# Optimization experiments

Hardware: AMD Instinct MI355X
Metric: run time of the kernel (lower is better)

The kernel has to match this reference:

```python
import jax, jax.numpy as jnp
import numpy as np

D_MODEL = 1024
N_HEADS = 16
D_HEAD = D_MODEL // N_HEADS
ROPE_BASE = 10000.0


def setup_inputs() -> dict:
    key = jax.random.key(0)
    k1, k2, k3, k4, k5 = jax.random.split(key, 5)
    std = 0.02 / np.sqrt(2 * 12)  # scaled_xavier with n_layers=12
    x = jax.random.normal(k1, (2, 2048, D_MODEL), dtype=jnp.float32)
    qkv_w = jax.random.normal(k2, (3 * D_MODEL, D_MODEL), dtype=jnp.float32) * std
    qkv_b = jnp.zeros((3 * D_MODEL,), dtype=jnp.float32)
    proj_w = jax.random.normal(k3, (D_MODEL, D_MODEL), dtype=jnp.float32) * std
    proj_b = jnp.zeros((D_MODEL,), dtype=jnp.float32)
    return {"x": x, "qkv_w": qkv_w, "qkv_b": qkv_b, "proj_w": proj_w, "proj_b": proj_b}


def _rope_cos_sin(seq_len, dtype):
    inv_freq = 1.0 / (ROPE_BASE ** (jnp.arange(0, D_HEAD, 2, dtype=jnp.float32) / D_HEAD))
    t = jnp.arange(seq_len, dtype=jnp.float32)
    freqs = jnp.einsum("t,d->td", t, inv_freq)          # [S, Dh/2]
    freqs = jnp.concatenate([freqs, freqs], axis=-1)      # [S, Dh]
    return jnp.cos(freqs).astype(dtype), jnp.sin(freqs).astype(dtype)


def _rotate_half(x):
    x1, x2 = jnp.split(x, 2, axis=-1)
    return jnp.concatenate([-x2, x1], axis=-1)


def reference(x, qkv_w, qkv_b, proj_w, proj_b):
    B, S, D = x.shape
    H, Dh = N_HEADS, D_HEAD
    scale = 1.0 / np.sqrt(Dh)

    qkv = x @ qkv_w.T + qkv_b                              # [B, S, 3D]
    qkv = qkv.reshape(B, S, 3, H, Dh)
    q = jnp.transpose(qkv[:, :, 0], (0, 2, 1, 3))          # [B, H, S, Dh]
    k = jnp.transpose(qkv[:, :, 1], (0, 2, 1, 3))
    v = jnp.transpose(qkv[:, :, 2], (0, 2, 1, 3))

    cos, sin = _rope_cos_sin(S, x.dtype)                   # [S, Dh]
    q = q * cos + _rotate_half(q) * sin
    k = k * cos + _rotate_half(k) * sin

    scores = jnp.einsum("bhsd,bhtd->bhst", q, k) * scale   # [B, H, S, S]
    causal = jnp.triu(jnp.ones((S, S), dtype=bool), k=1)
    neg = jnp.finfo(scores.dtype).min
    scores = jnp.where(causal[None, None], neg, scores)

    probs = jax.nn.softmax(scores, axis=-1)
    ctx = jnp.einsum("bhst,bhtd->bhsd", probs, v)          # [B, H, S, Dh]
    out = jnp.transpose(ctx, (0, 2, 1, 3)).reshape(B, S, D)
    out = out @ proj_w.T + proj_b
    return out
```

## Files before the change

### kernel.cpp

```cpp
#include <hip/hip_runtime.h>
#include <hip/hip_bf16.h>

#define BATCH 2
#define SEQ   2048
#define DMODEL 1024
#define NHEADS 16
#define DHEAD  64
#define MTOT   (BATCH * SEQ)
#define QKSTR  2048

typedef __attribute__((ext_vector_type(8))) short bf16x8;
typedef __attribute__((ext_vector_type(4))) float f32x4;

__device__ __forceinline__ void glds16(const void* g, void* l)
{
    __builtin_amdgcn_global_load_lds(
        (const __attribute__((address_space(1))) unsigned int*)g,
        (__attribute__((address_space(3))) unsigned int*)l, 16, 0, 0);
}

__global__ void cast_all_kernel(
    const float* __restrict__ a, __hip_bfloat16* __restrict__ oa, int na4,
    const float* __restrict__ b, __hip_bfloat16* __restrict__ ob, int nb4,
    const float* __restrict__ c, __hip_bfloat16* __restrict__ oc, int nc4)
{
    int i = blockIdx.x * blockDim.x + threadIdx.x;
    const float* src; __hip_bfloat16* dst; int j = i;
    if (j < na4) { src = a; dst = oa; }
    else {
        j -= na4;
        if (j < nb4) { src = b; dst = ob; }
        else {
            j -= nb4;
            if (j >= nc4) return;
            src = c; dst = oc;
        }
    }
    float4 v = ((const float4*)src)[j];
    __hip_bfloat16 tmp[4];
    tmp[0] = __float2bfloat16(v.x);
    tmp[1] = __float2bfloat16(v.y);
    tmp[2] = __float2bfloat16(v.z);
    tmp[3] = __float2bfloat16(v.w);
    *(uint2*)(dst + 4 * (size_t)j) = *(const uint2*)tmp;
}

#define GTM 128
#define GBK 64

__device__ __forceinline__ void store_out(float* p, float v) { *p = v; }
__device__ __forceinline__ void store_out(__hip_bfloat16* p, float v) { *p = __float2bfloat16(v); }

template <typename OutT, int MODE, int TN>
__global__ __launch_bounds__(256) void gemm_bias_kernel(
    const __hip_bfloat16* __restrict__ A, const __hip_bfloat16* __restrict__ W,
    const float* __restrict__ bias, OutT* __restrict__ out,
    __hip_bfloat16* __restrict__ vtg,
    int M, int N, int K)
{
    const int NI = TN / 32;
    const int bm = blockIdx.x * GTM;
    const int bn = blockIdx.y * TN;
    const int tid = threadIdx.x;
    const int wave = tid >> 6;
    const int lane = tid & 63;
    const int quad = lane >> 4;
    const int l16 = lane & 15;
    const int wm = (wave & 1) * 64;
    const int wn = (wave >> 1) * (TN / 2);

    __shared__ __hip_bfloat16 As[GTM * GBK];
    __shared__ __hip_bfloat16 Bs[TN * GBK];

    f32x4 acc[4][NI] = {};

    const int srow = lane >> 3;
    const int gc8 = (((lane & 7) ^ srow)) * 8;

    for (int kt = 0; kt < K; kt += GBK) {
#pragma unroll
        for (int t = 0; t < 4; t++) {
            int i = wave * 4 + t;
            glds16(A + (size_t)(bm + i * 8 + srow) * K + kt + gc8, As + i * 512);
        }
#pragma unroll
        for (int t = 0; t < TN / 32; t++) {
            int i = wave * (TN / 32) + t;
            glds16(W + (size_t)(bn + i * 8 + srow) * K + kt + gc8, Bs + i * 512);
        }
        __syncthreads();

#pragma unroll
        for (int kk = 0; kk < 2; kk++) {
            bf16x8 af[4], bfr[NI];
#pragma unroll
            for (int i = 0; i < 4; i++) {
                int ra = wm + i * 16 + l16;
                af[i] = *(const bf16x8*)(As + ra * 64 + (((kk << 2) + quad) ^ (ra & 7)) * 8);
            }
#pragma unroll
            for (int i = 0; i < NI; i++) {
                int rb = wn + i * 16 + l16;
                bfr[i] = *(const bf16x8*)(Bs + rb * 64 + (((kk << 2) + quad) ^ (rb & 7)) * 8);
            }
#pragma unroll
            for (int mi = 0; mi < 4; mi++)
#pragma unroll
                for (int ni = 0; ni < NI; ni++)
                    acc[mi][ni] = __builtin_amdgcn_mfma_f32_16x16x32_bf16(
                        af[mi], bfr[ni], acc[mi][ni], 0, 0, 0);
        }
        __syncthreads();
    }

    if (MODE == 1 && (bn + wn) < 2 * DMODEL) {
#pragma unroll
        for (int ni = 0; ni < 2; ni++) {
            int col = bn + wn + ni * 16 + l16;
            int i32 = col & 31;
            float invf = exp2f(-13.287712379549449f * (float)i32 * (1.0f / 32.0f));
            float b1 = bias[col], b2 = bias[col + 32];
#pragma unroll
            for (int mi = 0; mi < 4; mi++) {
#pragma unroll
                for (int r = 0; r < 4; r++) {
                    int row = bm + wm + mi * 16 + quad * 4 + r;
                    int s = row & (SEQ - 1);
                    float ang = (float)s * invf;
                    float sn, cs;
                    __sincosf(ang, &sn, &cs);
                    float x1 = acc[mi][ni][r] + b1;
                    float x2 = acc[mi][ni + 2][r] + b2;
                    store_out(&out[(size_t)row * QKSTR + col], x1 * cs - x2 * sn);
                    store_out(&out[(size_t)row * QKSTR + col + 32], x2 * cs + x1 * sn);
                }
            }
        }
    } else if (MODE == 1) {
#pragma unroll
        for (int ni = 0; ni < NI; ni++) {
            int colg = bn + wn + ni * 16 + l16;
            int vcol = colg - 2 * DMODEL;
            int hh = vcol >> 6, dh = vcol & 63;
            float bv = bias[colg];
#pragma unroll
            for (int mi = 0; mi < 4; mi++) {
                int row0 = bm + wm + mi * 16 + quad * 4;
                int bb = row0 >> 11;
                int ss = row0 & (SEQ - 1);
                __hip_bfloat16 tmp[4];
#pragma unroll
                for (int r = 0; r < 4; r++)
                    tmp[r] = __float2bfloat16(acc[mi][ni][r] + bv);
                *(uint2*)(vtg + (((size_t)bb * NHEADS + hh) * DHEAD + dh) * SEQ + ss) =
                    *(uint2*)tmp;
            }
        }
    } else {
#pragma unroll
        for (int mi = 0; mi < 4; mi++)
#pragma unroll
            for (int ni = 0; ni < NI; ni++) {
                int col = bn + wn + ni * 16 + l16;
                float bv = bias[col];
#pragma unroll
                for (int r = 0; r < 4; r++) {
                    int row = bm + wm + mi * 16 + quad * 4 + r;
                    store_out(&out[(size_t)row * N + col], acc[mi][ni][r] + bv);
                }
            }
    }
}

__global__ __launch_bounds__(512, 4) void flash_attn_mfma_kernel(
    const __hip_bfloat16* __restrict__ qkb,
    const __hip_bfloat16* __restrict__ vtg,
    __hip_bfloat16* __restrict__ ctx)
{
    const int bh = blockIdx.x;
    const int b = bh >> 4, h = bh & 15;
    const int y = blockIdx.y;
    const int qa = y, qb = 31 - y;
    const int tid = threadIdx.x;
    const int w = tid >> 6;
    const int lane = tid & 63;
    const int quad = lane >> 4;
    const int l16 = lane & 15;
    const int w4 = w & 3;
    const int qt = (w >> 2) ? qb : qa;

    __shared__ __hip_bfloat16 Ks[2][64 * 64];
    __shared__ __hip_bfloat16 Vt[2][64 * 64];
    __shared__ __hip_bfloat16 Ps[128 * 64];

    const __hip_bfloat16* qbase = qkb + (size_t)b * SEQ * QKSTR + h * DHEAD;
    const __hip_bfloat16* kbase = qbase + DMODEL;
    const __hip_bfloat16* vbase = vtg + (size_t)bh * DHEAD * SEQ;

    const __hip_bfloat16* qrow = qbase + (size_t)(qt * 64 + w4 * 16 + l16) * QKSTR;
    bf16x8 qf0 = *(const bf16x8*)(qrow + quad * 8);
    bf16x8 qf1 = *(const bf16x8*)(qrow + 32 + quad * 8);

    const int srow = lane >> 3;
    const int gc8 = ((lane & 7) ^ srow) * 8;
    const __hip_bfloat16* kg = kbase + (size_t)(w * 8 + srow) * QKSTR + gc8;
    const __hip_bfloat16* vg = vbase + (size_t)(w * 8 + srow) * SEQ + gc8;

    const int xr = l16 & 7;
    const int fo0 = l16 * 64 + ((quad ^ xr) << 3);
    const int fo1 = l16 * 64 + (((4 + quad) ^ xr) << 3);
    const int pband = w * 16;
    const int pfo0 = (pband + l16) * 64 + ((quad ^ xr) << 3);
    const int pfo1 = (pband + l16) * 64 + (((4 + quad) ^ xr) << 3);

    const short onev = (l16 == 0) ? (short)0x3F80 : (short)0;
    const bf16x8 ones = {onev, onev, onev, onev, onev, onev, onev, onev};

    glds16(kg, &Ks[0][w * 512]);
    glds16(vg, &Vt[0][w * 512]);

    f32x4 oacc[5] = {};

    for (int jt = 0; jt <= qb; jt++) {
        __syncthreads();
        const int cur = jt & 1;
        if (jt < qb) {
            glds16(kg + (size_t)(jt + 1) * 64 * QKSTR, &Ks[cur ^ 1][w * 512]);
            glds16(vg + (jt + 1) * 64, &Vt[cur ^ 1][w * 512]);
        }
        if (jt <= qt) {
            const __hip_bfloat16* ks = Ks[cur];
            const __hip_bfloat16* vs = Vt[cur];

            f32x4 s4[4] = {};
#pragma unroll
            for (int nt = 0; nt < 4; nt++)
                s4[nt] = __builtin_amdgcn_mfma_f32_16x16x32_bf16(
                    qf0, *(const bf16x8*)(ks + nt * 1024 + fo0), s4[nt], 0, 0, 0);
#pragma unroll
            for (int nt = 0; nt < 4; nt++)
                s4[nt] = __builtin_amdgcn_mfma_f32_16x16x32_bf16(
                    qf1, *(const bf16x8*)(ks + nt * 1024 + fo1), s4[nt], 0, 0, 0);

            const bool diag = (jt == qt);
#pragma unroll
            for (int nt = 0; nt < 4; nt++)
#pragma unroll
                for (int r = 0; r < 4; r++) {
                    float p = __expf(s4[nt][r] * 0.125f);
                    if (diag)
                        p = (nt * 16 + l16 <= w4 * 16 + quad * 4 + r) ? p : 0.f;
                    int rr = quad * 4 + r;
                    Ps[(pband + rr) * 64 +
                       (((nt * 2 + (l16 >> 3)) ^ (rr & 7)) << 3) + xr] =
                        __float2bfloat16(p);
                }

            bf16x8 pf0 = *(const bf16x8*)(Ps + pfo0);
            bf16x8 pf1 = *(const bf16x8*)(Ps + pfo1);
#pragma unroll
            for (int dt = 0; dt < 4; dt++)
                oacc[dt] = __builtin_amdgcn_mfma_f32_16x16x32_bf16(
                    pf0, *(const bf16x8*)(vs + dt * 1024 + fo0), oacc[dt], 0, 0, 0);
            oacc[4] = __builtin_amdgcn_mfma_f32_16x16x32_bf16(pf0, ones, oacc[4], 0, 0, 0);
#pragma unroll
            for (int dt = 0; dt < 4; dt++)
                oacc[dt] = __builtin_amdgcn_mfma_f32_16x16x32_bf16(
                    pf1, *(const bf16x8*)(vs + dt * 1024 + fo1), oacc[dt], 0, 0, 0);
            oacc[4] = __builtin_amdgcn_mfma_f32_16x16x32_bf16(pf1, ones, oacc[4], 0, 0, 0);
        }
    }

#pragma unroll
    for (int r = 0; r < 4; r++) {
        float lv = __shfl(oacc[4][r], lane & 48);
        float il = 1.0f / lv;
        int qg = qt * 64 + w4 * 16 + quad * 4 + r;
        __hip_bfloat16* op = ctx + (((size_t)b * SEQ + qg) * NHEADS + h) * DHEAD + l16;
#pragma unroll
        for (int dt = 0; dt < 4; dt++)
            op[dt * 16] = __float2bfloat16(oacc[dt][r] * il);
    }
}

extern "C" void kernel_launch(void* const* d_in, const int* in_sizes, int n_in,
                              void* d_out, int out_size, void* d_ws, size_t ws_size,
                              hipStream_t stream)
{
    const float* x      = (const float*)d_in[0];
    const float* qkv_w  = (const float*)d_in[1];
    const float* qkv_b  = (const float*)d_in[2];
    const float* proj_w = (const float*)d_in[3];
    const float* proj_b = (const float*)d_in[4];
    float* out = (float*)d_out;

    char* w = (char*)d_ws;
    __hip_bfloat16* qkb = (__hip_bfloat16*)w;  w += (size_t)MTOT * QKSTR * 2;
    __hip_bfloat16* vtg = (__hip_bfloat16*)w;  w += (size_t)MTOT * DMODEL * 2;
    __hip_bfloat16* ctx = (__hip_bfloat16*)w;  w += (size_t)MTOT * DMODEL * 2;
    __hip_bfloat16* xb  = (__hip_bfloat16*)w;  w += (size_t)MTOT * DMODEL * 2;
    __hip_bfloat16* wqk = (__hip_bfloat16*)w;  w += (size_t)3 * DMODEL * DMODEL * 2;
    __hip_bfloat16* wpr = (__hip_bfloat16*)w;

    const int na4 = MTOT * DMODEL / 4;
    const int nb4 = 3 * DMODEL * DMODEL / 4;
    const int nc4 = DMODEL * DMODEL / 4;

    cast_all_kernel<<<(na4 + nb4 + nc4 + 255) / 256, 256, 0, stream>>>(
        x, xb, na4, qkv_w, wqk, nb4, proj_w, wpr, nc4);

    gemm_bias_kernel<__hip_bfloat16, 1, 128>
        <<<dim3(MTOT / GTM, (3 * DMODEL) / 128), 256, 0, stream>>>(
        xb, wqk, qkv_b, qkb, vtg, MTOT, 3 * DMODEL, DMODEL);

    flash_attn_mfma_kernel<<<dim3(BATCH * NHEADS, 16), 512, 0, stream>>>(qkb, vtg, ctx);

    gemm_bias_kernel<float, 0, 64>
        <<<dim3(MTOT / GTM, DMODEL / 64), 256, 0, stream>>>(
        ctx, wpr, proj_b, out, nullptr, MTOT, DMODEL, DMODEL);
}
```

Baseline: 183.6 us.

## Double-buffer GEMM LDS tiles with K=32 steps to overlap loads and MFMA

The bias GEMM now stages A and W tiles in two LDS buffers of depth 32 along K, with a matching XOR swizzle. The loads for the next tile are issued before the MFMAs on the current tile, and one barrier per iteration replaces the previous two. This is meant to hide global-to-LDS latency behind compute. In exchange the K loop runs twice as many iterations with less work per barrier, and there is less MFMA work available to cover each load.

```diff
diff --git a/kernel.cpp b/kernel.cpp
--- a/kernel.cpp
+++ b/kernel.cpp
@@ -46,7 +46,6 @@
 }
 
 #define GTM 128
-#define GBK 64
 
 __device__ __forceinline__ void store_out(float* p, float v) { *p = v; }
 __device__ __forceinline__ void store_out(__hip_bfloat16* p, float v) { *p = __float2bfloat16(v); }
@@ -69,48 +68,73 @@
     const int wm = (wave & 1) * 64;
     const int wn = (wave >> 1) * (TN / 2);
 
-    __shared__ __hip_bfloat16 As[GTM * GBK];
-    __shared__ __hip_bfloat16 Bs[TN * GBK];
+    __shared__ __hip_bfloat16 As[2][GTM * 32];
+    __shared__ __hip_bfloat16 Bs[2][TN * 32];
 
     f32x4 acc[4][NI] = {};
 
-    const int srow = lane >> 3;
-    const int gc8 = (((lane & 7) ^ srow)) * 8;
-
-    for (int kt = 0; kt < K; kt += GBK) {
-#pragma unroll
-        for (int t = 0; t < 4; t++) {
-            int i = wave * 4 + t;
-            glds16(A + (size_t)(bm + i * 8 + srow) * K + kt + gc8, As + i * 512);
-        }
-#pragma unroll
-        for (int t = 0; t < TN / 32; t++) {
-            int i = wave * (TN / 32) + t;
-            glds16(W + (size_t)(bn + i * 8 + srow) * K + kt + gc8, Bs + i * 512);
-        }
+    const int r16 = lane >> 2;
+    const int gco = ((lane & 3) ^ (r16 & 3)) * 8;
+
+    const int fo = ((quad ^ (l16 & 3)) << 3);
+
+    const int niter = K >> 5;
+
+    {
+#pragma unroll
+        for (int c = 0; c < 2; c++) {
+            int br = wave * 32 + c * 16;
+            glds16(A + (size_t)(bm + br + r16) * K + gco, &As[0][br * 32]);
+        }
+        if (TN == 128) {
+#pragma unroll
+            for (int c = 0; c < 2; c++) {
+                int br = wave * 32 + c * 16;
+                glds16(W + (size_t)(bn + br + r16) * K + gco, &Bs[0][br * 32]);
+            }
+        } else {
+            int br = wave * 16;
+            glds16(W + (size_t)(bn + br + r16) * K + gco, &Bs[0][br * 32]);
+        }
+    }
+
+    for (int it = 0; it < niter; it++) {
         __syncthreads();
-
-#pragma unroll
-        for (int kk = 0; kk < 2; kk++) {
-            bf16x8 af[4], bfr[NI];
-#pragma unroll
-            for (int i = 0; i < 4; i++) {
-                int ra = wm + i * 16 + l16;
-                af[i] = *(const bf16x8*)(As + ra * 64 + (((kk << 2) + quad) ^ (ra & 7)) * 8);
-            }
-#pragma unroll
-            for (int i = 0; i < NI; i++) {
-                int rb = wn + i * 16 + l16;
-                bfr[i] = *(const bf16x8*)(Bs + rb * 64 + (((kk << 2) + quad) ^ (rb & 7)) * 8);
-            }
-#pragma unroll
-            for (int mi = 0; mi < 4; mi++)
-#pragma unroll
-                for (int ni = 0; ni < NI; ni++)
-                    acc[mi][ni] = __builtin_amdgcn_mfma_f32_16x16x32_bf16(
-                        af[mi], bfr[ni], acc[mi][ni], 0, 0, 0);
-        }
-        __syncthreads();
+        if (it + 1 < niter) {
+            int kt = (it + 1) << 5;
+            int nb = (it + 1) & 1;
+#pragma unroll
+            for (int c = 0; c < 2; c++) {
+                int br = wave * 32 + c * 16;
+                glds16(A + (size_t)(bm + br + r16) * K + kt + gco, &As[nb][br * 32]);
+            }
+            if (TN == 128) {
+#pragma unroll
+                for (int c = 0; c < 2; c++) {
+                    int br = wave * 32 + c * 16;
+                    glds16(W + (size_t)(bn + br + r16) * K + kt + gco, &Bs[nb][br * 32]);
+                }
+            } else {
+                int br = wave * 16;
+                glds16(W + (size_t)(bn + br + r16) * K + kt + gco, &Bs[nb][br * 32]);
+            }
+        }
+
+        const __hip_bfloat16* as = As[it & 1];
+        const __hip_bfloat16* bs = Bs[it & 1];
+        bf16x8 af[4], bfr[NI];
+#pragma unroll
+        for (int i = 0; i < 4; i++)
+            af[i] = *(const bf16x8*)(as + (wm + i * 16 + l16) * 32 + fo);
+#pragma unroll
+        for (int i = 0; i < NI; i++)
+            bfr[i] = *(const bf16x8*)(bs + (wn + i * 16 + l16) * 32 + fo);
+#pragma unroll
+        for (int mi = 0; mi < 4; mi++)
+#pragma unroll
+            for (int ni = 0; ni < NI; ni++)
+                acc[mi][ni] = __builtin_amdgcn_mfma_f32_16x16x32_bf16(
+                    af[mi], bfr[ni], acc[mi][ni], 0, 0, 0);
     }
 
     if (MODE == 1 && (bn + wn) < 2 * DMODEL) {
```

Result: slower. 191.4 us (+4.2%).

## Give each attention wave 32 query rows, halving grid and reusing K/V fragments

Applied to the files above, without the earlier changes.

The flash-attention kernel now processes 128-row query tiles per half-block, so each wave handles two 16-row query slices and reuses every K and V fragment loaded from LDS for both. The grid's y dimension drops from 16 to 8, the P staging buffer doubles, and the causal mask is applied per 16-row slice using a per-wave loop bound. This cuts LDS reads and K/V loads per query row, in exchange for more registers, lower occupancy (launch bounds 4 to 2), and fewer blocks, which may leave CUs underused.

```diff
diff --git a/kernel.cpp b/kernel.cpp
--- a/kernel.cpp
+++ b/kernel.cpp
@@ -172,7 +172,7 @@
     }
 }
 
-__global__ __launch_bounds__(512, 4) void flash_attn_mfma_kernel(
+__global__ __launch_bounds__(512, 2) void flash_attn_mfma_kernel(
     const __hip_bfloat16* __restrict__ qkb,
     const __hip_bfloat16* __restrict__ vtg,
     __hip_bfloat16* __restrict__ ctx)
@@ -180,26 +180,33 @@
     const int bh = blockIdx.x;
     const int b = bh >> 4, h = bh & 15;
     const int y = blockIdx.y;
-    const int qa = y, qb = 31 - y;
+    const int qa = y, qb = 15 - y;
     const int tid = threadIdx.x;
     const int w = tid >> 6;
     const int lane = tid & 63;
     const int quad = lane >> 4;
     const int l16 = lane & 15;
-    const int w4 = w & 3;
+    const int band = w & 3;
     const int qt = (w >> 2) ? qb : qa;
+    const int jmax_w = 2 * qt + (band >> 1);
+    const int jmax_b = 2 * qb + 1;
 
     __shared__ __hip_bfloat16 Ks[2][64 * 64];
     __shared__ __hip_bfloat16 Vt[2][64 * 64];
-    __shared__ __hip_bfloat16 Ps[128 * 64];
+    __shared__ __hip_bfloat16 Ps[256 * 64];
 
     const __hip_bfloat16* qbase = qkb + (size_t)b * SEQ * QKSTR + h * DHEAD;
     const __hip_bfloat16* kbase = qbase + DMODEL;
     const __hip_bfloat16* vbase = vtg + (size_t)bh * DHEAD * SEQ;
 
-    const __hip_bfloat16* qrow = qbase + (size_t)(qt * 64 + w4 * 16 + l16) * QKSTR;
-    bf16x8 qf0 = *(const bf16x8*)(qrow + quad * 8);
-    bf16x8 qf1 = *(const bf16x8*)(qrow + 32 + quad * 8);
+    bf16x8 qf[2][2];
+#pragma unroll
+    for (int mi = 0; mi < 2; mi++) {
+        const __hip_bfloat16* qr =
+            qbase + (size_t)(qt * 128 + band * 32 + mi * 16 + l16) * QKSTR;
+        qf[mi][0] = *(const bf16x8*)(qr + quad * 8);
+        qf[mi][1] = *(const bf16x8*)(qr + 32 + quad * 8);
+    }
 
     const int srow = lane >> 3;
     const int gc8 = ((lane & 7) ^ srow) * 8;
@@ -209,9 +216,7 @@
     const int xr = l16 & 7;
     const int fo0 = l16 * 64 + ((quad ^ xr) << 3);
     const int fo1 = l16 * 64 + (((4 + quad) ^ xr) << 3);
-    const int pband = w * 16;
-    const int pfo0 = (pband + l16) * 64 + ((quad ^ xr) << 3);
-    const int pfo1 = (pband + l16) * 64 + (((4 + quad) ^ xr) << 3);
+    const int pbase = w * 32;
 
     const short onev = (l16 == 0) ? (short)0x3F80 : (short)0;
     const bf16x8 ones = {onev, onev, onev, onev, onev, onev, onev, onev};
@@ -219,68 +224,91 @@
     glds16(kg, &Ks[0][w * 512]);
     glds16(vg, &Vt[0][w * 512]);
 
-    f32x4 oacc[5] = {};
-
-    for (int jt = 0; jt <= qb; jt++) {
+    f32x4 oacc[2][5] = {};
+
+    for (int jt = 0; jt <= jmax_b; jt++) {
         __syncthreads();
         const int cur = jt & 1;
-        if (jt < qb) {
+        if (jt < jmax_b) {
             glds16(kg + (size_t)(jt + 1) * 64 * QKSTR, &Ks[cur ^ 1][w * 512]);
             glds16(vg + (jt + 1) * 64, &Vt[cur ^ 1][w * 512]);
         }
-        if (jt <= qt) {
+        if (jt <= jmax_w) {
             const __hip_bfloat16* ks = Ks[cur];
             const __hip_bfloat16* vs = Vt[cur];
 
-            f32x4 s4[4] = {};
-#pragma unroll
-            for (int nt = 0; nt < 4; nt++)
-                s4[nt] = __builtin_amdgcn_mfma_f32_16x16x32_bf16(
-                    qf0, *(const bf16x8*)(ks + nt * 1024 + fo0), s4[nt], 0, 0, 0);
-#pragma unroll
-            for (int nt = 0; nt < 4; nt++)
-                s4[nt] = __builtin_amdgcn_mfma_f32_16x16x32_bf16(
-                    qf1, *(const bf16x8*)(ks + nt * 1024 + fo1), s4[nt], 0, 0, 0);
-
-            const bool diag = (jt == qt);
-#pragma unroll
-            for (int nt = 0; nt < 4; nt++)
-#pragma unroll
-                for (int r = 0; r < 4; r++) {
-                    float p = __expf(s4[nt][r] * 0.125f);
-                    if (diag)
-                        p = (nt * 16 + l16 <= w4 * 16 + quad * 4 + r) ? p : 0.f;
-                    int rr = quad * 4 + r;
-                    Ps[(pband + rr) * 64 +
-                       (((nt * 2 + (l16 >> 3)) ^ (rr & 7)) << 3) + xr] =
-                        __float2bfloat16(p);
+            f32x4 s4[2][4] = {};
+#pragma unroll
+            for (int kk = 0; kk < 2; kk++) {
+                const int fo = kk ? fo1 : fo0;
+                bf16x8 kf[4];
+#pragma unroll
+                for (int nt = 0; nt < 4; nt++)
+                    kf[nt] = *(const bf16x8*)(ks + nt * 1024 + fo);
+#pragma unroll
+                for (int mi = 0; mi < 2; mi++)
+#pragma unroll
+                    for (int nt = 0; nt < 4; nt++)
+                        s4[mi][nt] = __builtin_amdgcn_mfma_f32_16x16x32_bf16(
+                            qf[mi][kk], kf[nt], s4[mi][nt], 0, 0, 0);
+            }
+
+            const int k0 = jt * 64;
+#pragma unroll
+            for (int mi = 0; mi < 2; mi++) {
+                const int qmin = qt * 128 + band * 32 + mi * 16;
+                const bool needmask = (k0 + 63) > qmin;
+#pragma unroll
+                for (int nt = 0; nt < 4; nt++)
+#pragma unroll
+                    for (int r = 0; r < 4; r++) {
+                        float p = __expf(s4[mi][nt][r] * 0.125f);
+                        if (needmask)
+                            p = (k0 + nt * 16 + l16 <= qmin + quad * 4 + r) ? p : 0.f;
+                        int rr = quad * 4 + r;
+                        Ps[(pbase + mi * 16 + rr) * 64 +
+                           (((nt * 2 + (l16 >> 3)) ^ (rr & 7)) << 3) + xr] =
+                            __float2bfloat16(p);
+                    }
+            }
+
+#pragma unroll
+            for (int kk = 0; kk < 2; kk++) {
+                const int fo = kk ? fo1 : fo0;
+                bf16x8 pf[2];
+#pragma unroll
+                for (int mi = 0; mi < 2; mi++)
+                    pf[mi] = *(const bf16x8*)(Ps + (pbase + mi * 16 + l16) * 64 +
+                                              ((((kk << 2) + quad) ^ xr) << 3));
+#pragma unroll
+                for (int dt = 0; dt < 4; dt++) {
+                    bf16x8 vf = *(const bf16x8*)(vs + dt * 1024 + fo);
+#pragma unroll
+                    for (int mi = 0; mi < 2; mi++)
+                        oacc[mi][dt] = __builtin_amdgcn_mfma_f32_16x16x32_bf16(
+                            pf[mi], vf, oacc[mi][dt], 0, 0, 0);
                 }
-
-            bf16x8 pf0 = *(const bf16x8*)(Ps + pfo0);
-            bf16x8 pf1 = *(const bf16x8*)(Ps + pfo1);
+#pragma unroll
+                for (int mi = 0; mi < 2; mi++)
+                    oacc[mi][4] = __builtin_amdgcn_mfma_f32_16x16x32_bf16(
+                        pf[mi], ones, oacc[mi][4], 0, 0, 0);
+            }
+        }
+    }
+
+#pragma unroll
+    for (int mi = 0; mi < 2; mi++)
+#pragma unroll
+        for (int r = 0; r < 4; r++) {
+            float lv = __shfl(oacc[mi][4][r], lane & 48);
+            float il = 1.0f / lv;
+            int qg = qt * 128 + band * 32 + mi * 16 + quad * 4 + r;
+            __hip_bfloat16* op =
+                ctx + (((size_t)b * SEQ + qg) * NHEADS + h) * DHEAD + l16;
 #pragma unroll
             for (int dt = 0; dt < 4; dt++)
-                oacc[dt] = __builtin_amdgcn_mfma_f32_16x16x32_bf16(
-                    pf0, *(const bf16x8*)(vs + dt * 1024 + fo0), oacc[dt], 0, 0, 0);
-            oacc[4] = __builtin_amdgcn_mfma_f32_16x16x32_bf16(pf0, ones, oacc[4], 0, 0, 0);
-#pragma unroll
-            for (int dt = 0; dt < 4; dt++)
-                oacc[dt] = __builtin_amdgcn_mfma_f32_16x16x32_bf16(
-                    pf1, *(const bf16x8*)(vs + dt * 1024 + fo1), oacc[dt], 0, 0, 0);
-            oacc[4] = __builtin_amdgcn_mfma_f32_16x16x32_bf16(pf1, ones, oacc[4], 0, 0, 0);
-        }
-    }
-
-#pragma unroll
-    for (int r = 0; r < 4; r++) {
-        float lv = __shfl(oacc[4][r], lane & 48);
-        float il = 1.0f / lv;
-        int qg = qt * 64 + w4 * 16 + quad * 4 + r;
-        __hip_bfloat16* op = ctx + (((size_t)b * SEQ + qg) * NHEADS + h) * DHEAD + l16;
-#pragma unroll
-        for (int dt = 0; dt < 4; dt++)
-            op[dt * 16] = __float2bfloat16(oacc[dt][r] * il);
-    }
+                op[dt * 16] = __float2bfloat16(oacc[mi][dt][r] * il);
+        }
 }
 
 extern "C" void kernel_launch(void* const* d_in, const int* in_sizes, int n_in,
@@ -313,7 +341,7 @@
         <<<dim3(MTOT / GTM, (3 * DMODEL) / 128), 256, 0, stream>>>(
         xb, wqk, qkv_b, qkb, vtg, MTOT, 3 * DMODEL, DMODEL);
 
-    flash_attn_mfma_kernel<<<dim3(BATCH * NHEADS, 16), 512, 0, stream>>>(qkb, vtg, ctx);
+    flash_attn_mfma_kernel<<<dim3(BATCH * NHEADS, 8), 512, 0, stream>>>(qkb, vtg, ctx);
 
     gemm_bias_kernel<float, 0, 64>
         <<<dim3(MTOT / GTM, DMODEL / 64), 256, 0, stream>>>(
```

After: 202.5 us. 10.3% more time.
